# Optimization experiments

Measured on AMD Instinct MI355X. Metric: run time of the kernel, lower is better.

Reference implementation:

```python
import jax, jax.numpy as jnp
import numpy as np


def setup_inputs() -> dict:
    key = jax.random.key(0)
    k1, k2, k3, k4, k5 = jax.random.split(key, 5)
    B, S, K, N, G = 4, 2048, 4096, 4096, 64  # G = group_size -> num_groups = K // G = 64
    x = jax.random.normal(k1, (B, S, K), dtype=jnp.float32)
    # int2 codes stored one-per-int8 slot (low 2 bits valid); use int32 container
    weight_q = jax.random.randint(k2, (N, K), 0, 4, dtype=jnp.int32)
    scale = jax.random.uniform(k3, (N, K // G), dtype=jnp.float32) * 0.05 + 0.01
    zp = jax.random.uniform(k4, (N, K // G), dtype=jnp.float32) * 3.0
    bias = jax.random.normal(k5, (N,), dtype=jnp.float32)
    return {"x": x, "weight_q": weight_q, "scale": scale, "zp": zp, "bias": bias}


def _dequant(weight_q, scale, zp):
    # weight_q: [N, K] int codes in [0,4); scale/zp: [N, num_groups]
    N, K = weight_q.shape
    num_groups = scale.shape[1]
    gs = K // num_groups  # group_size
    q = weight_q.astype(jnp.float32).reshape(N, num_groups, gs)
    w = (q - zp[:, :, None]) * scale[:, :, None]
    return w.reshape(N, K)


def reference(x, weight_q, scale, zp, bias):
    # asymm_qw2_gemm: out = x @ dequant(W)^T + bias
    w = _dequant(weight_q, scale, zp)            # [N, K]
    out = jnp.einsum('bsk,nk->bsn', x, w)        # [B, S, N]
    return out + bias
```

## Files before the change

### kernel.cpp

```cpp
#include <hip/hip_runtime.h>
#include <stdint.h>


typedef __attribute__((ext_vector_type(4))) float  f32x4;
typedef __attribute__((ext_vector_type(4))) int    i32x4;
typedef __attribute__((ext_vector_type(8))) __bf16 bf16x8;
typedef __attribute__((ext_vector_type(4))) unsigned short u16x4;

__device__ __forceinline__ unsigned short f2bf(float f) {
  unsigned u = __builtin_bit_cast(unsigned, f);
  u += 0x7fffu + ((u >> 16) & 1u);
  return (unsigned short)(u >> 16);
}

__device__ __forceinline__ void async16(const void* g, void* l) {
  __builtin_amdgcn_global_load_lds(
      (const __attribute__((address_space(1))) unsigned int*)g,
      (__attribute__((address_space(3))) unsigned int*)l, 16, 0, 0);
}

__global__ __launch_bounds__(256) void prep_kernel(
    const float* __restrict__ x, unsigned short* __restrict__ xb, int xchunks,
    const int* __restrict__ wq, const float* __restrict__ scale,
    const float* __restrict__ zp, unsigned short* __restrict__ wb,
    int wchunks, int K, int G) {
  int xblocks = (xchunks + 255) >> 8;
  if ((int)blockIdx.x < xblocks) {
    int i = blockIdx.x * 256 + threadIdx.x;
    if (i >= xchunks) return;
    f32x4 a = ((const f32x4*)x)[i];
    u16x4 o;
    o[0] = f2bf(a[0]); o[1] = f2bf(a[1]); o[2] = f2bf(a[2]); o[3] = f2bf(a[3]);
    *(u16x4*)(xb + (size_t)i * 4) = o;
  } else {
    int i = (blockIdx.x - xblocks) * 256 + threadIdx.x;
    if (i >= wchunks) return;
    int k4 = i * 4;
    int n = k4 / K, kk = k4 % K;
    int ng = K / G;
    int g = kk / G;
    float s = scale[(size_t)n * ng + g];
    float b = -zp[(size_t)n * ng + g] * s;
    i32x4 qv = ((const i32x4*)wq)[i];
    u16x4 o;
    o[0] = f2bf((float)qv[0] * s + b); o[1] = f2bf((float)qv[1] * s + b);
    o[2] = f2bf((float)qv[2] * s + b); o[3] = f2bf((float)qv[3] * s + b);
    *(u16x4*)(wb + (size_t)i * 4) = o;
  }
}

#define BM 128
#define BN 128
#define BK 32

__global__ __launch_bounds__(256, 2) void gemm_bt_kernel(
    const unsigned short* __restrict__ A,
    const unsigned short* __restrict__ B,
    const float* __restrict__ bias,
    float* __restrict__ C, int M, int N, int K) {
  __shared__ unsigned short As[BM * BK];
  __shared__ unsigned short Bs[BN * BK];

  const int tid  = threadIdx.x;
  const int lane = tid & 63;
  const int wave = tid >> 6;
  const int wm = wave >> 1, wn = wave & 1;
  const int q = lane >> 4, r = lane & 15;
  const int m0 = blockIdx.y * BM;
  const int n0 = blockIdx.x * BN;

  const int srow = tid >> 2, schunk = tid & 3;
  const int gchunk = schunk ^ ((srow >> 1) & 3);
  const unsigned short* aG0 = A + (size_t)(m0 + srow) * K      + gchunk * 8;
  const unsigned short* aG1 = A + (size_t)(m0 + 64 + srow) * K + gchunk * 8;
  const unsigned short* bG0 = B + (size_t)(n0 + srow) * K      + gchunk * 8;
  const unsigned short* bG1 = B + (size_t)(n0 + 64 + srow) * K + gchunk * 8;
  unsigned short* aL0 = &As[tid * 8];
  unsigned short* aL1 = &As[2048 + tid * 8];
  unsigned short* bL0 = &Bs[tid * 8];
  unsigned short* bL1 = &Bs[2048 + tid * 8];

  const int qc = (q ^ ((r >> 1) & 3)) * 8;

  f32x4 acc[4][4] = {};

#pragma unroll 1
  for (int kk = 0; kk < K; kk += BK) {
    async16(aG0 + kk, aL0);
    async16(aG1 + kk, aL1);
    async16(bG0 + kk, bL0);
    async16(bG1 + kk, bL1);
    __syncthreads();

    bf16x8 af[4], bf[4];
#pragma unroll
    for (int i = 0; i < 4; ++i) {
      af[i] = *(const bf16x8*)&As[(wm * 64 + i * 16 + r) * BK + qc];
      bf[i] = *(const bf16x8*)&Bs[(wn * 64 + i * 16 + r) * BK + qc];
    }
#pragma unroll
    for (int i = 0; i < 4; ++i)
#pragma unroll
      for (int j = 0; j < 4; ++j)
        acc[i][j] = __builtin_amdgcn_mfma_f32_16x16x32_bf16(af[i], bf[j], acc[i][j], 0, 0, 0);
    __syncthreads();
  }

  float bv[4];
#pragma unroll
  for (int j = 0; j < 4; ++j) bv[j] = bias[n0 + wn * 64 + j * 16 + r];
#pragma unroll
  for (int i = 0; i < 4; ++i) {
    int mbase = m0 + wm * 64 + i * 16 + q * 4;
#pragma unroll
    for (int e = 0; e < 4; ++e) {
      float* crow = C + (size_t)(mbase + e) * N + n0 + wn * 64 + r;
#pragma unroll
      for (int j = 0; j < 4; ++j)
        crow[j * 16] = acc[i][j][e] + bv[j];
    }
  }
}

__global__ __launch_bounds__(256) void naive_kernel(
    const float* __restrict__ x, const int* __restrict__ wq,
    const float* __restrict__ scale, const float* __restrict__ zp,
    const float* __restrict__ bias, float* __restrict__ out,
    int M, int N, int K, int G) {
  int idx = blockIdx.x * 256 + threadIdx.x;
  if (idx >= M * N) return;
  int m = idx / N, n = idx % N;
  const float* xr = x + (size_t)m * K;
  const int* wr = wq + (size_t)n * K;
  int ng = K / G;
  float acc = 0.f;
  for (int g = 0; g < ng; ++g) {
    float s = scale[(size_t)n * ng + g];
    float b = -zp[(size_t)n * ng + g] * s;
    for (int k = 0; k < G; ++k)
      acc += xr[g * G + k] * ((float)wr[g * G + k] * s + b);
  }
  out[idx] = acc + bias[n];
}

extern "C" void kernel_launch(void* const* d_in, const int* in_sizes, int n_in,
                              void* d_out, int out_size, void* d_ws, size_t ws_size,
                              hipStream_t stream) {
  const float* x     = (const float*)d_in[0];
  const int*   wq    = (const int*)d_in[1];
  const float* scale = (const float*)d_in[2];
  const float* zp    = (const float*)d_in[3];
  const float* bias  = (const float*)d_in[4];
  float* out = (float*)d_out;

  const int N  = in_sizes[4];
  const int K  = in_sizes[1] / N;
  const int ng = in_sizes[2] / N;
  const int G  = K / ng;
  const int M  = in_sizes[0] / K;

  size_t xb_bytes = (size_t)M * K * 2;
  size_t wb_bytes = (size_t)N * K * 2;
  if (ws_size < xb_bytes + wb_bytes) {
    int total = M * N;
    naive_kernel<<<dim3((total + 255) / 256), dim3(256), 0, stream>>>(
        x, wq, scale, zp, bias, out, M, N, K, G);
    return;
  }

  unsigned short* xb = (unsigned short*)d_ws;
  unsigned short* wb = (unsigned short*)((char*)d_ws + xb_bytes);

  int xchunks = M * K / 4;
  int wchunks = N * K / 4;
  int xblocks = (xchunks + 255) / 256;
  int wblocks = (wchunks + 255) / 256;
  prep_kernel<<<dim3(xblocks + wblocks), dim3(256), 0, stream>>>(
      x, xb, xchunks, wq, scale, zp, wb, wchunks, K, G);

  dim3 grid(N / BN, M / BM);
  gemm_bt_kernel<<<grid, dim3(256), 0, stream>>>(xb, wb, bias, out, M, N, K);
}
```

Before: 561.4 us.

## Use single-wave 64x64 GEMM blocks with double-buffered async LDS prefetch

The 256-thread 128x128 GEMM block becomes a single 64-lane wave computing a 64x64 tile. Global-to-LDS copies for the next K slice are issued into a second buffer before the current slice's MFMAs run, and barriers are replaced by waitcnt instructions. This removes block-level __syncthreads and overlaps load latency with compute. In exchange, each tile is reused across fewer outputs, so the A and B tiles are fetched from L2 about twice as often, and the grid has four times as many blocks.

```diff
diff --git a/kernel.cpp b/kernel.cpp
--- a/kernel.cpp
+++ b/kernel.cpp
@@ -49,72 +49,78 @@
   }
 }
 
-#define BM 128
-#define BN 128
-#define BK 32
-
-__global__ __launch_bounds__(256, 2) void gemm_bt_kernel(
+__global__ __launch_bounds__(64) void gemm_bt_kernel(
     const unsigned short* __restrict__ A,
     const unsigned short* __restrict__ B,
     const float* __restrict__ bias,
     float* __restrict__ C, int M, int N, int K) {
-  __shared__ unsigned short As[BM * BK];
-  __shared__ unsigned short Bs[BN * BK];
+  __shared__ __align__(16) unsigned short lds[8192];
 
-  const int tid  = threadIdx.x;
-  const int lane = tid & 63;
-  const int wave = tid >> 6;
-  const int wm = wave >> 1, wn = wave & 1;
-  const int q = lane >> 4, r = lane & 15;
-  const int m0 = blockIdx.y * BM;
-  const int n0 = blockIdx.x * BN;
+  const int l = threadIdx.x;
+  const int q = l >> 4, r = l & 15;
+  const int m0 = blockIdx.y * 64;
+  const int n0 = blockIdx.x * 64;
 
-  const int srow = tid >> 2, schunk = tid & 3;
-  const int gchunk = schunk ^ ((srow >> 1) & 3);
-  const unsigned short* aG0 = A + (size_t)(m0 + srow) * K      + gchunk * 8;
-  const unsigned short* aG1 = A + (size_t)(m0 + 64 + srow) * K + gchunk * 8;
-  const unsigned short* bG0 = B + (size_t)(n0 + srow) * K      + gchunk * 8;
-  const unsigned short* bG1 = B + (size_t)(n0 + 64 + srow) * K + gchunk * 8;
-  unsigned short* aL0 = &As[tid * 8];
-  unsigned short* aL1 = &As[2048 + tid * 8];
-  unsigned short* bL0 = &Bs[tid * 8];
-  unsigned short* bL1 = &Bs[2048 + tid * 8];
+  const int srow = l >> 2;
+  const int gchunk = (l & 3) ^ ((l >> 3) & 3);
+  const unsigned short* aG = A + (size_t)(m0 + srow) * K + gchunk * 8;
+  const unsigned short* bG = B + (size_t)(n0 + srow) * K + gchunk * 8;
+  const size_t rstep = (size_t)16 * K;
+
+  unsigned short* cur = lds;
+  unsigned short* nxt = lds + 4096;
 
   const int qc = (q ^ ((r >> 1) & 3)) * 8;
+
+#pragma unroll
+  for (int j = 0; j < 4; ++j) {
+    async16(aG + (size_t)j * rstep, cur + j * 512 + l * 8);
+    async16(bG + (size_t)j * rstep, cur + 2048 + j * 512 + l * 8);
+  }
 
   f32x4 acc[4][4] = {};
 
 #pragma unroll 1
-  for (int kk = 0; kk < K; kk += BK) {
-    async16(aG0 + kk, aL0);
-    async16(aG1 + kk, aL1);
-    async16(bG0 + kk, bL0);
-    async16(bG1 + kk, bL1);
-    __syncthreads();
+  for (int kk = 0; kk < K; kk += 32) {
+    asm volatile("s_waitcnt lgkmcnt(0)" ::: "memory");
+
+    int kn = kk + 32; if (kn == K) kn = 0;
+    const unsigned short* aGk = aG + kn;
+    const unsigned short* bGk = bG + kn;
+#pragma unroll
+    for (int j = 0; j < 4; ++j) {
+      async16(aGk + (size_t)j * rstep, nxt + j * 512 + l * 8);
+      async16(bGk + (size_t)j * rstep, nxt + 2048 + j * 512 + l * 8);
+    }
+
+    asm volatile("s_waitcnt vmcnt(8)" ::: "memory");
 
     bf16x8 af[4], bf[4];
 #pragma unroll
     for (int i = 0; i < 4; ++i) {
-      af[i] = *(const bf16x8*)&As[(wm * 64 + i * 16 + r) * BK + qc];
-      bf[i] = *(const bf16x8*)&Bs[(wn * 64 + i * 16 + r) * BK + qc];
+      af[i] = *(const bf16x8*)&cur[(i * 16 + r) * 32 + qc];
+      bf[i] = *(const bf16x8*)&cur[2048 + (i * 16 + r) * 32 + qc];
     }
 #pragma unroll
     for (int i = 0; i < 4; ++i)
 #pragma unroll
       for (int j = 0; j < 4; ++j)
         acc[i][j] = __builtin_amdgcn_mfma_f32_16x16x32_bf16(af[i], bf[j], acc[i][j], 0, 0, 0);
-    __syncthreads();
+
+    unsigned short* t = cur; cur = nxt; nxt = t;
   }
+
+  asm volatile("s_waitcnt vmcnt(0)" ::: "memory");
 
   float bv[4];
 #pragma unroll
-  for (int j = 0; j < 4; ++j) bv[j] = bias[n0 + wn * 64 + j * 16 + r];
+  for (int j = 0; j < 4; ++j) bv[j] = bias[n0 + j * 16 + r];
 #pragma unroll
   for (int i = 0; i < 4; ++i) {
-    int mbase = m0 + wm * 64 + i * 16 + q * 4;
+    int mbase = m0 + i * 16 + q * 4;
 #pragma unroll
     for (int e = 0; e < 4; ++e) {
-      float* crow = C + (size_t)(mbase + e) * N + n0 + wn * 64 + r;
+      float* crow = C + (size_t)(mbase + e) * N + n0 + r;
 #pragma unroll
       for (int j = 0; j < 4; ++j)
         crow[j * 16] = acc[i][j][e] + bv[j];
@@ -178,6 +184,6 @@
   prep_kernel<<<dim3(xblocks + wblocks), dim3(256), 0, stream>>>(
       x, xb, xchunks, wq, scale, zp, wb, wchunks, K, G);
 
-  dim3 grid(N / BN, M / BM);
-  gemm_bt_kernel<<<grid, dim3(256), 0, stream>>>(xb, wb, bias, out, M, N, K);
+  dim3 grid(N / 64, M / 64);
+  gemm_bt_kernel<<<grid, dim3(64), 0, stream>>>(xb, wb, bias, out, M, N, K);
 }
```

Result: slower. 1.005 ms (+79.0%).

## Double-buffer LDS tiles to prefetch next K-slice during MFMA compute

Applied to the files above, without the earlier changes.

Doubles the LDS allocation into two buffers and issues async global-to-LDS loads for the next K tile before computing on the current one. Manual s_waitcnt vmcnt(4) and s_barrier replace the __syncthreads pairs, so memory latency can overlap with the MFMA work. A wasted wraparound prefetch happens on the last iteration, and the doubled LDS use may reduce occupancy.

```diff
diff --git a/kernel.cpp b/kernel.cpp
--- a/kernel.cpp
+++ b/kernel.cpp
@@ -49,25 +49,20 @@
   }
 }
 
-#define BM 128
-#define BN 128
-#define BK 32
-
 __global__ __launch_bounds__(256, 2) void gemm_bt_kernel(
     const unsigned short* __restrict__ A,
     const unsigned short* __restrict__ B,
     const float* __restrict__ bias,
     float* __restrict__ C, int M, int N, int K) {
-  __shared__ unsigned short As[BM * BK];
-  __shared__ unsigned short Bs[BN * BK];
+  __shared__ __align__(16) unsigned short lds[16384];
 
   const int tid  = threadIdx.x;
   const int lane = tid & 63;
   const int wave = tid >> 6;
   const int wm = wave >> 1, wn = wave & 1;
   const int q = lane >> 4, r = lane & 15;
-  const int m0 = blockIdx.y * BM;
-  const int n0 = blockIdx.x * BN;
+  const int m0 = blockIdx.y * 128;
+  const int n0 = blockIdx.x * 128;
 
   const int srow = tid >> 2, schunk = tid & 3;
   const int gchunk = schunk ^ ((srow >> 1) & 3);
@@ -75,36 +70,49 @@
   const unsigned short* aG1 = A + (size_t)(m0 + 64 + srow) * K + gchunk * 8;
   const unsigned short* bG0 = B + (size_t)(n0 + srow) * K      + gchunk * 8;
   const unsigned short* bG1 = B + (size_t)(n0 + 64 + srow) * K + gchunk * 8;
-  unsigned short* aL0 = &As[tid * 8];
-  unsigned short* aL1 = &As[2048 + tid * 8];
-  unsigned short* bL0 = &Bs[tid * 8];
-  unsigned short* bL1 = &Bs[2048 + tid * 8];
+
+  unsigned short* cur = lds;
+  unsigned short* nxt = lds + 8192;
 
   const int qc = (q ^ ((r >> 1) & 3)) * 8;
+
+  async16(aG0, cur + tid * 8);
+  async16(aG1, cur + 2048 + tid * 8);
+  async16(bG0, cur + 4096 + tid * 8);
+  async16(bG1, cur + 6144 + tid * 8);
 
   f32x4 acc[4][4] = {};
 
 #pragma unroll 1
-  for (int kk = 0; kk < K; kk += BK) {
-    async16(aG0 + kk, aL0);
-    async16(aG1 + kk, aL1);
-    async16(bG0 + kk, bL0);
-    async16(bG1 + kk, bL1);
-    __syncthreads();
+  for (int kk = 0; kk < K; kk += 32) {
+    int kn = kk + 32; if (kn == K) kn = 0;
+    async16(aG0 + kn, nxt + tid * 8);
+    async16(aG1 + kn, nxt + 2048 + tid * 8);
+    async16(bG0 + kn, nxt + 4096 + tid * 8);
+    async16(bG1 + kn, nxt + 6144 + tid * 8);
+
+    asm volatile("s_waitcnt vmcnt(4)" ::: "memory");
+    asm volatile("s_barrier" ::: "memory");
 
     bf16x8 af[4], bf[4];
 #pragma unroll
     for (int i = 0; i < 4; ++i) {
-      af[i] = *(const bf16x8*)&As[(wm * 64 + i * 16 + r) * BK + qc];
-      bf[i] = *(const bf16x8*)&Bs[(wn * 64 + i * 16 + r) * BK + qc];
+      af[i] = *(const bf16x8*)&cur[(wm * 64 + i * 16 + r) * 32 + qc];
+      bf[i] = *(const bf16x8*)&cur[4096 + (wn * 64 + i * 16 + r) * 32 + qc];
     }
+    asm volatile("s_waitcnt lgkmcnt(0)" ::: "memory");
+    asm volatile("s_barrier" ::: "memory");
+
 #pragma unroll
     for (int i = 0; i < 4; ++i)
 #pragma unroll
       for (int j = 0; j < 4; ++j)
         acc[i][j] = __builtin_amdgcn_mfma_f32_16x16x32_bf16(af[i], bf[j], acc[i][j], 0, 0, 0);
-    __syncthreads();
+
+    unsigned short* t = cur; cur = nxt; nxt = t;
   }
+
+  asm volatile("s_waitcnt vmcnt(0)" ::: "memory");
 
   float bv[4];
 #pragma unroll
@@ -178,6 +186,6 @@
   prep_kernel<<<dim3(xblocks + wblocks), dim3(256), 0, stream>>>(
       x, xb, xchunks, wq, scale, zp, wb, wchunks, K, G);
 
-  dim3 grid(N / BN, M / BM);
+  dim3 grid(N / 128, M / 128);
   gemm_bt_kernel<<<grid, dim3(256), 0, stream>>>(xb, wb, bias, out, M, N, K);
 }
```

Result: slower. 579.0 us (+3.1%).
